# Kernel optimization log

Hardware: AMD Instinct MI355X
Metric: run time of the kernel (lower is better)

## Reference

```python
import jax, jax.numpy as jnp
import numpy as np

B, L = 256, 8192
DIM, NPAT, HIST, WIN = 256, 64, 32, 8


def setup_inputs() -> dict:
    key = jax.random.key(0)
    ks = jax.random.split(key, 6)
    return {
        "x": jax.random.normal(ks[0], (B, L), dtype=jnp.float32),
        "avg_init": jax.random.normal(ks[1], (B, NPAT), dtype=jnp.float32),
        "conv_w": jax.random.normal(ks[2], (DIM, 1, HIST), dtype=jnp.float32) * 0.1,
        "conv_b": jax.random.normal(ks[3], (DIM,), dtype=jnp.float32) * 0.1,
        "keys_w": jax.random.normal(ks[4], (NPAT, DIM), dtype=jnp.float32) * 0.1,
        "shapes_w": jax.random.normal(ks[5], (WIN, NPAT), dtype=jnp.float32) * 0.1,
    }


def reference(x, avg_init, conv_w, conv_b, keys_w, shapes_w):
    b, l = x.shape
    n_pat = keys_w.shape[0]
    hist = conv_w.shape[2]
    win = shapes_w.shape[0]

    # randn avg_scores, centered (module draws fresh randn each forward; we take it as input)
    avg0 = avg_init - jnp.mean(avg_init, axis=-1, keepdims=True)

    padded = jnp.pad(x, ((0, 0), (hist - 1, 0)))[:, None, :]  # [B,1,L+hist-1]
    out = jax.lax.conv_general_dilated(
        padded, conv_w, window_strides=(win,), padding="VALID",
        dimension_numbers=("NCH", "OIH", "NCH"))
    out = out + conv_b[None, :, None]                     # [B,dim,T]
    out = jnp.transpose(out, (2, 0, 1))                   # [T,B,dim]

    # relu6(keys(out)) -> attn scores [T,B,n_pat]
    scores = jnp.clip(jnp.einsum("tbd,pd->tbp", out, keys_w), 0.0, 6.0)

    # sequential balanced-routing scan over T with running average scores
    def step(avg, score):                                 # avg,score: [B,n_pat]
        idx = jnp.argmax(score - avg, axis=-1)
        prob = jax.nn.one_hot(idx, n_pat, dtype=score.dtype)
        return avg + prob - 1.0 / n_pat, prob

    _, probs = jax.lax.scan(step, avg0, scores)           # probs: [T,B,n_pat]
    probs = jnp.transpose(probs, (1, 0, 2))               # [B,T,n_pat]

    signal = jnp.einsum("btp,wp->btw", probs, shapes_w).reshape(b, -1)[:, :l]
    return jax.nn.relu(signal - x)
```

## Files before the change

### kernel.cpp

```cpp
#include <hip/hip_runtime.h>


constexpr int Bb = 256, Ll = 8192, DIMc = 256, NPAT = 64, HIST = 32, WINc = 8;
constexpr int Tt = Ll / WINc;
constexpr int TC = 32;
constexpr int NC = Tt / TC;

#define DPP_MAXF(m, ctrl, rmask)                                               \
  do {                                                                         \
    int _mi = __float_as_int(m);                                               \
    int _ti = __builtin_amdgcn_update_dpp(_mi, _mi, (ctrl), (rmask), 0xF, false); \
    (m) = fmaxf((m), __int_as_float(_ti));                                     \
  } while (0)

__global__ void precompute_kernel(const float* __restrict__ conv_w,
                                  const float* __restrict__ conv_b,
                                  const float* __restrict__ keys_w,
                                  float* __restrict__ wsf) {
  int gid = blockIdx.x * blockDim.x + threadIdx.x;
  if (gid < NPAT * HIST) {
    int p = gid >> 5, h = gid & 31;
    float acc = 0.f;
    for (int d = 0; d < DIMc; ++d)
      acc = fmaf(keys_w[p * DIMc + d], conv_w[d * HIST + h], acc);
    wsf[(h >> 2) * (NPAT * 4) + p * 4 + (h & 3)] = acc;
  } else if (gid < NPAT * HIST + NPAT) {
    int p = gid - NPAT * HIST;
    float acc = 0.f;
    for (int d = 0; d < DIMc; ++d)
      acc = fmaf(keys_w[p * DIMc + d], conv_b[d], acc);
    wsf[NPAT * HIST + p] = acc;
  }
}

__global__ __launch_bounds__(256) void shaper_kernel(
    const float* __restrict__ x, const float* __restrict__ avg_init,
    const float* __restrict__ shapes_w, const float* __restrict__ wsf,
    float* __restrict__ out) {
  __shared__ __align__(16) float xpad[HIST - 1 + Ll + 1];
  __shared__ float scb[2][TC * NPAT];
  __shared__ int   idxb[Tt];
  __shared__ float shp[WINc * NPAT];

  const int b    = blockIdx.x;
  const int tid  = threadIdx.x;
  const int wid  = tid >> 6;
  const int lane = tid & 63;
  const float* xrow = x + (size_t)b * Ll;

  if (tid < HIST - 1) xpad[tid] = 0.f;
  for (int i = tid; i < Ll; i += 256) xpad[HIST - 1 + i] = xrow[i];
  for (int i = tid; i < WINc * NPAT; i += 256) shp[i] = shapes_w[i];

  float4 w2v[8];
  float  b2 = 0.f;
  if (wid > 0) {
    const float4* w2g = (const float4*)wsf;
#pragma unroll
    for (int h4 = 0; h4 < 8; ++h4) w2v[h4] = w2g[h4 * 64 + lane];
    b2 = wsf[NPAT * HIST + lane];
  }
  float av = 0.f;
  if (wid == 0) {
    const float* ai = avg_init + (size_t)b * NPAT;
    float s = 0.f;
    for (int j = 0; j < NPAT; ++j) s += ai[j];
    av = ai[lane] - s * (1.0f / NPAT);
  }
  __syncthreads();

  auto fill = [&](int c, float* __restrict__ sb) {
    int base = c * TC;
    for (int tl = wid - 1; tl < TC; tl += 3) {
      int t = base + tl;
      const float4* xw = (const float4*)(xpad + t * WINc);
      float acc = b2;
#pragma unroll
      for (int h4 = 0; h4 < 8; ++h4) {
        float4 xv = xw[h4];
        float4 wv = w2v[h4];
        acc = fmaf(xv.x, wv.x, acc);
        acc = fmaf(xv.y, wv.y, acc);
        acc = fmaf(xv.z, wv.z, acc);
        acc = fmaf(xv.w, wv.w, acc);
      }
      float sc = fminf(fmaxf(acc, 0.f), 6.f);
      sb[tl * NPAT + lane] = sc;
    }
  };

  auto scan16 = [&](const float* r, int tbase) {
#pragma unroll
    for (int i = 0; i < 16; ++i) {
      float v = r[i] - av;
      float m = v;
      DPP_MAXF(m, 0xB1, 0xF);
      DPP_MAXF(m, 0x4E, 0xF);
      DPP_MAXF(m, 0x141, 0xF);
      DPP_MAXF(m, 0x140, 0xF);
      DPP_MAXF(m, 0x142, 0xA);
      DPP_MAXF(m, 0x143, 0xC);
      float gmax = __int_as_float(
          __builtin_amdgcn_readlane(__float_as_int(m), 63));
      unsigned long long mk = __ballot(v == gmax);
      int winner = __ffsll(mk) - 1;
      if (lane == 0) idxb[tbase + i] = winner;
      float prob = (lane == winner) ? 1.0f : 0.0f;
      av = (av + prob) - (1.0f / NPAT);
    }
  };

  if (wid > 0) fill(0, scb[0]);
  __syncthreads();

  for (int c = 0; c < NC; ++c) {
    if (wid == 0) {
      float* sb = scb[c & 1];
      float r0[16], r1[16];
#pragma unroll
      for (int i = 0; i < 16; ++i) r0[i] = sb[i * NPAT + lane];
#pragma unroll
      for (int i = 0; i < 16; ++i) r1[i] = sb[(16 + i) * NPAT + lane];
      scan16(r0, c * TC);
      scan16(r1, c * TC + 16);
    } else if (c + 1 < NC) {
      fill(c + 1, scb[(c + 1) & 1]);
    }
    __syncthreads();
  }

  float4* outv = (float4*)(out + (size_t)b * Ll);
#pragma unroll
  for (int k = 0; k < 8; ++k) {
    int i4 = k * 256 + tid;
    int l0 = i4 * 4;
    int t  = l0 >> 3;
    int w0 = l0 & 7;
    int p  = idxb[t];
    float4 o;
    o.x = fmaxf(shp[(w0 + 0) * NPAT + p] - xpad[HIST - 1 + l0 + 0], 0.f);
    o.y = fmaxf(shp[(w0 + 1) * NPAT + p] - xpad[HIST - 1 + l0 + 1], 0.f);
    o.z = fmaxf(shp[(w0 + 2) * NPAT + p] - xpad[HIST - 1 + l0 + 2], 0.f);
    o.w = fmaxf(shp[(w0 + 3) * NPAT + p] - xpad[HIST - 1 + l0 + 3], 0.f);
    outv[i4] = o;
  }
}

extern "C" void kernel_launch(void* const* d_in, const int* in_sizes, int n_in,
                              void* d_out, int out_size, void* d_ws, size_t ws_size,
                              hipStream_t stream) {
  const float* x        = (const float*)d_in[0];
  const float* avg_init = (const float*)d_in[1];
  const float* conv_w   = (const float*)d_in[2];
  const float* conv_b   = (const float*)d_in[3];
  const float* keys_w   = (const float*)d_in[4];
  const float* shapes_w = (const float*)d_in[5];
  float* wsf = (float*)d_ws;

  precompute_kernel<<<9, 256, 0, stream>>>(conv_w, conv_b, keys_w, wsf);
  shaper_kernel<<<Bb, 256, 0, stream>>>(x, avg_init, shapes_w, wsf,
                                        (float*)d_out);
}
```

Measured before the change: 201.8 us.

## Shorten scan dependency chain with speculative next-step values and batch index writes

Result: faster. 186.7 us (-7.5%).

```diff
diff --git a/kernel.cpp b/kernel.cpp
--- a/kernel.cpp
+++ b/kernel.cpp
@@ -5,6 +5,7 @@
 constexpr int Tt = Ll / WINc;
 constexpr int TC = 32;
 constexpr int NC = Tt / TC;
+constexpr float CINV = 1.0f / 64.0f;
 
 #define DPP_MAXF(m, ctrl, rmask)                                               \
   do {                                                                         \
@@ -13,23 +14,37 @@
     (m) = fmaxf((m), __int_as_float(_ti));                                     \
   } while (0)
 
-__global__ void precompute_kernel(const float* __restrict__ conv_w,
-                                  const float* __restrict__ conv_b,
-                                  const float* __restrict__ keys_w,
-                                  float* __restrict__ wsf) {
-  int gid = blockIdx.x * blockDim.x + threadIdx.x;
-  if (gid < NPAT * HIST) {
-    int p = gid >> 5, h = gid & 31;
-    float acc = 0.f;
-    for (int d = 0; d < DIMc; ++d)
-      acc = fmaf(keys_w[p * DIMc + d], conv_w[d * HIST + h], acc);
-    wsf[(h >> 2) * (NPAT * 4) + p * 4 + (h & 3)] = acc;
-  } else if (gid < NPAT * HIST + NPAT) {
-    int p = gid - NPAT * HIST;
-    float acc = 0.f;
-    for (int d = 0; d < DIMc; ++d)
-      acc = fmaf(keys_w[p * DIMc + d], conv_b[d], acc);
-    wsf[NPAT * HIST + p] = acc;
+__global__ __launch_bounds__(256) void precompute_kernel(
+    const float* __restrict__ conv_w, const float* __restrict__ conv_b,
+    const float* __restrict__ keys_w, float* __restrict__ wsf) {
+  __shared__ float part[8][32];
+  __shared__ float bred[4];
+  const int p = blockIdx.x;
+  const int t = threadIdx.x;
+  const int h = t & 31, g = t >> 5;
+  const float* kwp = keys_w + (size_t)p * DIMc;
+
+  float acc = 0.f;
+#pragma unroll
+  for (int dd = 0; dd < 32; ++dd) {
+    int d = g * 32 + dd;
+    acc = fmaf(kwp[d], conv_w[d * HIST + h], acc);
+  }
+  part[g][h] = acc;
+
+  float bp = kwp[t] * conv_b[t];
+#pragma unroll
+  for (int off = 32; off; off >>= 1) bp += __shfl_down(bp, off);
+  if ((t & 63) == 0) bred[t >> 6] = bp;
+  __syncthreads();
+
+  if (t < 32) {
+    float s = 0.f;
+#pragma unroll
+    for (int gg = 0; gg < 8; ++gg) s += part[gg][t];
+    wsf[(t >> 2) * (NPAT * 4) + p * 4 + (t & 3)] = s;
+  } else if (t == 32) {
+    wsf[NPAT * HIST + p] = (bred[0] + bred[1]) + (bred[2] + bred[3]);
   }
 }
 
@@ -49,7 +64,16 @@
   const float* xrow = x + (size_t)b * Ll;
 
   if (tid < HIST - 1) xpad[tid] = 0.f;
-  for (int i = tid; i < Ll; i += 256) xpad[HIST - 1 + i] = xrow[i];
+  {
+    const float4* xv4 = (const float4*)xrow;
+#pragma unroll
+    for (int k = 0; k < 8; ++k) {
+      int i4 = k * 256 + tid;
+      float4 v = xv4[i4];
+      float* dst = xpad + HIST - 1 + i4 * 4;
+      dst[0] = v.x; dst[1] = v.y; dst[2] = v.z; dst[3] = v.w;
+    }
+  }
   for (int i = tid; i < WINc * NPAT; i += 256) shp[i] = shapes_w[i];
 
   float4 w2v[8];
@@ -84,15 +108,22 @@
         acc = fmaf(xv.z, wv.z, acc);
         acc = fmaf(xv.w, wv.w, acc);
       }
-      float sc = fminf(fmaxf(acc, 0.f), 6.f);
-      sb[tl * NPAT + lane] = sc;
+      sb[tl * NPAT + lane] = fminf(fmaxf(acc, 0.f), 6.f);
     }
   };
 
-  auto scan16 = [&](const float* r, int tbase) {
+  auto scan_chunk = [&](const float* __restrict__ sb, int tbase) {
+    float r[TC];
 #pragma unroll
-    for (int i = 0; i < 16; ++i) {
-      float v = r[i] - av;
+    for (int i = 0; i < TC; ++i) r[i] = sb[i * NPAT + lane];
+    float v = r[0] - av;
+    int stash = 0;
+#pragma unroll
+    for (int i = 0; i < TC; ++i) {
+      float t0 = av - CINV;
+      float t1 = (av + 1.0f) - CINV;
+      float vA = 0.f, vB = 0.f;
+      if (i + 1 < TC) { vA = r[i + 1] - t0; vB = r[i + 1] - t1; }
       float m = v;
       DPP_MAXF(m, 0xB1, 0xF);
       DPP_MAXF(m, 0x4E, 0xF);
@@ -104,10 +135,12 @@
           __builtin_amdgcn_readlane(__float_as_int(m), 63));
       unsigned long long mk = __ballot(v == gmax);
       int winner = __ffsll(mk) - 1;
-      if (lane == 0) idxb[tbase + i] = winner;
-      float prob = (lane == winner) ? 1.0f : 0.0f;
-      av = (av + prob) - (1.0f / NPAT);
+      stash = (lane == i) ? winner : stash;
+      bool win = (lane == winner);
+      av = win ? t1 : t0;
+      if (i + 1 < TC) v = win ? vB : vA;
     }
+    if (lane < TC) idxb[tbase + lane] = stash;
   };
 
   if (wid > 0) fill(0, scb[0]);
@@ -115,14 +148,7 @@
 
   for (int c = 0; c < NC; ++c) {
     if (wid == 0) {
-      float* sb = scb[c & 1];
-      float r0[16], r1[16];
-#pragma unroll
-      for (int i = 0; i < 16; ++i) r0[i] = sb[i * NPAT + lane];
-#pragma unroll
-      for (int i = 0; i < 16; ++i) r1[i] = sb[(16 + i) * NPAT + lane];
-      scan16(r0, c * TC);
-      scan16(r1, c * TC + 16);
+      scan_chunk(scb[c & 1], c * TC);
     } else if (c + 1 < NC) {
       fill(c + 1, scb[(c + 1) & 1]);
     }
@@ -157,7 +183,7 @@
   const float* shapes_w = (const float*)d_in[5];
   float* wsf = (float*)d_ws;
 
-  precompute_kernel<<<9, 256, 0, stream>>>(conv_w, conv_b, keys_w, wsf);
+  precompute_kernel<<<NPAT, 256, 0, stream>>>(conv_w, conv_b, keys_w, wsf);
   shaper_kernel<<<Bb, 256, 0, stream>>>(x, avg_init, shapes_w, wsf,
                                         (float*)d_out);
 }
```
